# Performance work log

Hardware: AMD Instinct MI355X
Metric: run time of the kernel (lower is better)

## Reference

```python
import jax, jax.numpy as jnp
import numpy as np

# dims (match init_kwargs / input_specs)
B, T = 32, 512
DIM, DEPTH, HEADS, NB_FEAT, N_MASKS = 256, 6, 8, 128, 4
DIM_HEAD = DIM // HEADS  # 32
FF_MULT = 4
KERNEL_EPS = 1e-4


def _orth_proj(key, m, d):
    # FAVOR+ gaussian orthogonal random features: stacked QR blocks, row norms from fresh gaussians
    nb = m // d
    keys = jax.random.split(key, nb + 1)
    blocks = []
    for i in range(nb):
        g = jax.random.normal(keys[i], (d, d))
        q, _ = jnp.linalg.qr(g)
        blocks.append(q.T)
    proj = jnp.concatenate(blocks, axis=0)  # (m, d)
    norms = jnp.linalg.norm(jax.random.normal(keys[-1], (m, d)), axis=-1)
    return (proj * norms[:, None]).astype(jnp.float32)


def setup_inputs() -> dict:
    key = jax.random.key(0)
    ks = jax.random.split(key, 12)
    init = lambda k, sh: (jax.random.normal(k, sh, dtype=jnp.float32) * 0.02)
    L = DEPTH
    return {
        "mel": jax.random.normal(ks[0], (B, DIM, T), dtype=jnp.float32),
        "proj": _orth_proj(ks[1], NB_FEAT, DIM_HEAD),
        "ln1_g": jnp.ones((L, DIM), jnp.float32), "ln1_b": jnp.zeros((L, DIM), jnp.float32),
        "Wq": init(ks[2], (L, DIM, DIM)), "Wk": init(ks[3], (L, DIM, DIM)),
        "Wv": init(ks[4], (L, DIM, DIM)),
        "Wo": init(ks[5], (L, DIM, DIM)), "bo": jnp.zeros((L, DIM), jnp.float32),
        "ln2_g": jnp.ones((L, DIM), jnp.float32), "ln2_b": jnp.zeros((L, DIM), jnp.float32),
        "W1": init(ks[6], (L, DIM, FF_MULT * DIM)), "b1": jnp.zeros((L, FF_MULT * DIM), jnp.float32),
        "W2": init(ks[7], (L, FF_MULT * DIM, DIM)), "b2": jnp.zeros((L, DIM), jnp.float32),
        "Wm": init(ks[8], (DIM, N_MASKS)), "bm": jnp.zeros((N_MASKS,), jnp.float32),
    }


def _ln(x, g, b):
    mu = jnp.mean(x, -1, keepdims=True)
    var = jnp.var(x, -1, keepdims=True)
    return (x - mu) * jax.lax.rsqrt(var + 1e-5) * g + b


def _softmax_kernel(x, proj, is_query):
    # x: (B,H,N,dh), proj: (m,dh)
    dn = x.shape[-1] ** -0.25
    ratio = proj.shape[0] ** -0.5
    xd = jnp.einsum('bhnd,md->bhnm', x * dn, proj)
    diag = 0.5 * jnp.sum(jnp.square(x * dn), axis=-1, keepdims=True)
    if is_query:
        mx = jnp.max(xd, axis=-1, keepdims=True)
    else:
        mx = jnp.max(xd, axis=(-1, -2), keepdims=True)
    return ratio * (jnp.exp(xd - diag - mx) + KERNEL_EPS)


def _split_heads(x):
    b, n, _ = x.shape
    return x.reshape(b, n, HEADS, DIM_HEAD).transpose(0, 2, 1, 3)  # (B,H,N,dh)


def _forward(mel, proj, ln1_g, ln1_b, Wq, Wk, Wv, Wo, bo, ln2_g, ln2_b, W1, b1, W2, b2, Wm, bm):
    x = jnp.transpose(mel, (0, 2, 1))  # (B, T, DIM)
    for l in range(DEPTH):
        # --- FAVOR+ self-attention (pre-LN, non-causal linear attention) ---
        h = _ln(x, ln1_g[l], ln1_b[l])
        q = _split_heads(h @ Wq[l])
        k = _split_heads(h @ Wk[l])
        v = _split_heads(h @ Wv[l])
        qp = _softmax_kernel(q, proj, True)   # (B,H,T,m)
        kp = _softmax_kernel(k, proj, False)  # (B,H,T,m)
        ctx = jnp.einsum('bhnm,bhnd->bhmd', kp, v)          # (B,H,m,dh)
        o = jnp.einsum('bhnm,bhmd->bhnd', qp, ctx)          # (B,H,T,dh)
        denom = jnp.einsum('bhnm,bhm->bhn', qp, kp.sum(axis=2))
        o = o / denom[..., None]
        o = o.transpose(0, 2, 1, 3).reshape(x.shape[0], x.shape[1], DIM)
        x = x + o @ Wo[l] + bo[l]
        h = _ln(x, ln2_g[l], ln2_b[l])
        x = x + jax.nn.gelu(h @ W1[l] + b1[l]) @ W2[l] + b2[l]
    masks = x @ Wm + bm                  # (B, T, M)
    return jnp.transpose(masks, (0, 2, 1))  # (B, M, T)


def reference(mel, proj, ln1_g, ln1_b, Wq, Wk, Wv, Wo, bo, ln2_g, ln2_b, W1, b1, W2, b2, Wm, bm):
    return _forward(mel, proj, ln1_g, ln1_b, Wq, Wk, Wv, Wo, bo, ln2_g, ln2_b, W1, b1, W2, b2, Wm, bm)
```

## Files before the change

kernel.cpp:

```cpp
#include <hip/hip_runtime.h>
#include <math.h>

#define B 32
#define T 512
#define D 256
#define H 8
#define DH 32
#define MF 128
#define NLAYER 6
#define FF 1024
#define NM 4
#define BT (B*T)
#define BH (B*H)

#define DN2H 0.08838834764831845f
#define DNS  0.4204482076268573f
#define RATIO 0.08838834764831845f
#define KEPS 1e-4f

typedef __attribute__((ext_vector_type(8))) short short8;
typedef __attribute__((ext_vector_type(4))) float f32x4;

#define MFMA(a, b, c) __builtin_amdgcn_mfma_f32_16x16x32_bf16(a, b, c, 0, 0, 0)

#define SWZG(l) (((((l) & 3) + (((l) >> 3) & 3)) & 3) * 8)
#define RS(li, gi) (((((gi) - ((li) >> 1)) & 3)) * 8)

__device__ __forceinline__ ushort f2b(float x) {
  union { float f; unsigned u; } c; c.f = x;
  unsigned r = (c.u + 0x7FFFu + ((c.u >> 16) & 1u)) >> 16;
  return (ushort)r;
}
__device__ __forceinline__ float bf2f(ushort u) {
  union { unsigned u; float f; } c; c.u = ((unsigned)u) << 16;
  return c.f;
}
__device__ __forceinline__ void gload16(const ushort* g, ushort* l) {
  __builtin_amdgcn_global_load_lds((const __attribute__((address_space(1))) void*)g,
                                   (__attribute__((address_space(3))) void*)l, 16, 0, 0);
}

__global__ void transpose_mel(const float* __restrict__ mel, float* __restrict__ x) {
  __shared__ float tile[32][33];
  int b = blockIdx.z;
  int d0 = blockIdx.y * 32, t0 = blockIdx.x * 32;
  int tx = threadIdx.x, ty = threadIdx.y;
  #pragma unroll
  for (int i = 0; i < 32; i += 8)
    tile[ty + i][tx] = mel[(b * D + d0 + ty + i) * T + t0 + tx];
  __syncthreads();
  #pragma unroll
  for (int i = 0; i < 32; i += 8)
    x[(b * T + t0 + ty + i) * D + d0 + tx] = tile[tx][ty + i];
}

__global__ void wtrans(const float* __restrict__ W, ushort* __restrict__ WT,
                       int K, int N, size_t lin, size_t lout) {
  __shared__ float tile[32][33];
  int l = blockIdx.z;
// ... 11 lines not shown
}

__global__ void proj_conv(const float* __restrict__ proj, ushort* __restrict__ projd) {
  int e = blockIdx.x * 256 + threadIdx.x;
  if (e < MF * DH) projd[e] = f2b(proj[e] * DNS);
}

__global__ __launch_bounds__(256) void ln_kernel(const float* __restrict__ x, const float* __restrict__ g,
                          const float* __restrict__ bb, ushort* __restrict__ y) {
  int row = blockIdx.x * 4 + (threadIdx.x >> 6);
  int lane = threadIdx.x & 63;
  const float4 v = ((const float4*)(x + (size_t)row * D))[lane];
  float s = v.x + v.y + v.z + v.w;
  #pragma unroll
  for (int off = 32; off; off >>= 1) s += __shfl_down(s, off);
  s = __shfl(s, 0);
  float mu = s * (1.0f / 256.0f);
  float dx = v.x - mu, dy = v.y - mu, dz = v.z - mu, dw = v.w - mu;
  float q = dx * dx + dy * dy + dz * dz + dw * dw;
  #pragma unroll
  for (int off = 32; off; off >>= 1) q += __shfl_down(q, off);
  q = __shfl(q, 0);
  float rstd = rsqrtf(q * (1.0f / 256.0f) + 1e-5f);
  const float4 gg = ((const float4*)g)[lane];
  const float4 be = ((const float4*)bb)[lane];
  ushort4 o;
  o.x = f2b(dx * rstd * gg.x + be.x);
  o.y = f2b(dy * rstd * gg.y + be.y);
  o.z = f2b(dz * rstd * gg.z + be.z);
  o.w = f2b(dw * rstd * gg.w + be.w);
  ((ushort4*)(y + (size_t)row * D))[lane] = o;
}

template<int EPI, int BM>
__global__ __launch_bounds__(256) void gemm_bf16(
    const ushort* __restrict__ A, const ushort* __restrict__ BTm,
    const float* __restrict__ bias,
    ushort* __restrict__ outB,
    ushort* __restrict__ qo, ushort* __restrict__ ko, ushort* __restrict__ vT,
    int N, int K) {
  constexpr int MFR = BM / 32;
  __shared__ __align__(16) ushort Al[2][BM * 32];
  __shared__ __align__(16) ushort Bl[2][128 * 32];
  int tid = threadIdx.x;
  int wave = tid >> 6, lane = tid & 63;
  int wr = wave >> 1, wc = wave & 1;
  int gi = lane >> 4, li = lane & 15;
  int lrow = lane >> 2, lkb = SWZG(lane);
  int row0 = blockIdx.y * BM, col0 = blockIdx.x * 128;
  f32x4 acc[MFR][4] = {};

  auto stage = [&](int buf, int kk) {
    #pragma unroll
    for (int i = 0; i < BM / 64; i++) {
      int chunk = wave * (BM / 64) + i;
      gload16(&A[(size_t)(row0 + chunk * 16 + lrow) * K + kk + lkb], &Al[buf][chunk * 512]);
    }
    #pragma unroll
    for (int i = 0; i < 2; i++) {
      int chunk = wave * 2 + i;
      gload16(&BTm[(size_t)(col0 + chunk * 16 + lrow) * K + kk + lkb], &Bl[buf][chunk * 512]);
    }
  };

  stage(0, 0);
  __syncthreads();
  int cur = 0;
  for (int k0 = 0; k0 < K; k0 += 32, cur ^= 1) {
    if (k0 + 32 < K) stage(cur ^ 1, k0 + 32);
    short8 a[MFR], b[4];
    #pragma unroll
    for (int m = 0; m < MFR; m++)
      a[m] = *(const short8*)&Al[cur][(wr * (MFR * 16) + m * 16 + li) * 32 + RS(li, gi)];
    #pragma unroll
    for (int n = 0; n < 4; n++)
      b[n] = *(const short8*)&Bl[cur][(wc * 64 + n * 16 + li) * 32 + RS(li, gi)];
    #pragma unroll
    for (int m = 0; m < MFR; m++)
      #pragma unroll
      for (int n = 0; n < 4; n++)
        acc[m][n] = MFMA(a[m], b[n], acc[m][n]);
    __syncthreads();
  }
  #pragma unroll
  for (int m = 0; m < MFR; m++) {
    int rbase = row0 + wr * (MFR * 16) + m * 16 + gi * 4;
    #pragma unroll
    for (int n = 0; n < 4; n++) {
      int col = col0 + wc * 64 + n * 16 + li;
      f32x4 v = acc[m][n];
      if (EPI == 2) {
        float bs = bias[col];
        #pragma unroll
        for (int r = 0; r < 4; r++) {
          float u = v[r] + bs;
          float p = u + 0.044715f * u * u * u;
          float gel = u / (1.0f + __expf(-1.5957691216057308f * p));
          outB[(size_t)(rbase + r) * N + col] = f2b(gel);
        }
      } else {
        if (col < 256) {
          #pragma unroll
          for (int r = 0; r < 4; r++) qo[(size_t)(rbase + r) * 256 + col] = f2b(v[r]);
        } else if (col < 512) {
          #pragma unroll
          for (int r = 0; r < 4; r++) ko[(size_t)(rbase + r) * 256 + col - 256] = f2b(v[r]);
        } else {
          int b_ = rbase >> 9, t = rbase & 511;
          int hh = (col - 512) >> 5, d = (col - 512) & 31;
          ushort4 pk;
          pk.x = f2b(v[0]); pk.y = f2b(v[1]); pk.z = f2b(v[2]); pk.w = f2b(v[3]);
          *(ushort4*)&vT[((size_t)((b_ * 8 + hh) * 32 + d)) * 512 + t] = pk;
        }
      }
    }
  }
}

__global__ __launch_bounds__(256) void ctx_fused(
    const ushort* __restrict__ kb, const ushort* __restrict__ projd,
    const ushort* __restrict__ vT, ushort* __restrict__ Bmat) {
  __shared__ __align__(16) ushort Kl[512 * 32];
  __shared__ __align__(16) ushort Pl[128 * 32];
  __shared__ __align__(16) ushort Sl[2][128 * 40];
  __shared__ __align__(16) ushort Bvl[2][32 * 32];
  __shared__ float dg_s[512];
  __shared__ float red_s[256];
  int bh = blockIdx.x;
  int b = bh >> 3, h = bh & 7;
  int tid = threadIdx.x, wave = tid >> 6, lane = tid & 63;
  int gi = lane >> 4, li = lane & 15;
  int lrow = lane >> 2, lkb = (lane & 3) * 8;
  const ushort* Kg = kb + (size_t)(b * 512) * 256 + h * 32;
  const ushort* Vg = vT + (size_t)bh * 32 * 512;
  #pragma unroll
  for (int i = 0; i < 8; i++) {
    int chunk = wave * 8 + i;
    gload16(&Kg[(size_t)(chunk * 16 + lrow) * 256 + lkb], &Kl[chunk * 512]);
  }
  #pragma unroll
  for (int i = 0; i < 2; i++) {
    int chunk = wave * 2 + i;
    gload16(&projd[(chunk * 16 + lrow) * 32 + lkb], &Pl[chunk * 512]);
  }
  __syncthreads();
  #pragma unroll
  for (int i = 0; i < 2; i++) {
    int t = tid * 2 + i;
    const ushort* kr = &Kl[t * 32];
    float s = 0.f;
    #pragma unroll
    for (int j = 0; j < 32; j++) { float v = bf2f(kr[j]); s += v * v; }
    dg_s[t] = DN2H * s;
  }
  short8 bp0 = *(const short8*)&Pl[(wave * 32 + li) * 32 + gi * 8];
  short8 bp1 = *(const short8*)&Pl[(wave * 32 + 16 + li) * 32 + gi * 8];
  float smax = -1e30f;
  for (int c = 0; c < 16; c++) {
    int t0c = c * 32;
    short8 a0 = *(const short8*)&Kl[(t0c + li) * 32 + gi * 8];
    short8 a1 = *(const short8*)&Kl[(t0c + 16 + li) * 32 + gi * 8];
    f32x4 s00 = {}, s01 = {}, s10 = {}, s11 = {};
    s00 = MFMA(a0, bp0, s00); s01 = MFMA(a0, bp1, s01);
    s10 = MFMA(a1, bp0, s10); s11 = MFMA(a1, bp1, s11);
    #pragma unroll
    for (int r = 0; r < 4; r++)
      smax = fmaxf(smax, fmaxf(fmaxf(s00[r], s01[r]), fmaxf(s10[r], s11[r])));
  }
  red_s[tid] = smax;
  __syncthreads();
  for (int s = 128; s; s >>= 1) {
    if (tid < s) red_s[tid] = fmaxf(red_s[tid], red_s[tid + s]);
    __syncthreads();
  }
  float km = red_s[0];
  f32x4 cacc[2][2] = {};
  float ks0 = 0.f, ks1 = 0.f;
  int cur = 0;
  for (int c = 0; c < 16; c++, cur ^= 1) {
    int t0c = c * 32;
    if (wave < 2)
      gload16(&Vg[(size_t)(wave * 16 + lrow) * 512 + t0c + lkb], &Bvl[cur][wave * 512]);
    short8 a0 = *(const short8*)&Kl[(t0c + li) * 32 + gi * 8];
    short8 a1 = *(const short8*)&Kl[(t0c + 16 + li) * 32 + gi * 8];
    f32x4 s00 = {}, s01 = {}, s10 = {}, s11 = {};
    s00 = MFMA(a0, bp0, s00); s01 = MFMA(a0, bp1, s01);
    s10 = MFMA(a1, bp0, s10); s11 = MFMA(a1, bp1, s11);
    ushort4 w00, w01, w10, w11;
    #pragma unroll
    for (int r = 0; r < 4; r++) {
      float d0 = dg_s[t0c + gi * 4 + r];
      float d1 = dg_s[t0c + 16 + gi * 4 + r];
      float k00 = RATIO * (__expf(s00[r] - d0 - km) + KEPS);
      float k01 = RATIO * (__expf(s01[r] - d0 - km) + KEPS);
      float k10 = RATIO * (__expf(s10[r] - d1 - km) + KEPS);
      float k11 = RATIO * (__expf(s11[r] - d1 - km) + KEPS);
      ks0 += k00 + k10; ks1 += k01 + k11;
      ((ushort*)&w00)[r] = f2b(k00); ((ushort*)&w01)[r] = f2b(k01);
      ((ushort*)&w10)[r] = f2b(k10); ((ushort*)&w11)[r] = f2b(k11);
    }
    *(ushort4*)&Sl[cur][(wave * 32 + li) * 40 + gi * 4]           = w00;
    *(ushort4*)&Sl[cur][(wave * 32 + 16 + li) * 40 + gi * 4]      = w01;
    *(ushort4*)&Sl[cur][(wave * 32 + li) * 40 + 16 + gi * 4]      = w10;
    *(ushort4*)&Sl[cur][(wave * 32 + 16 + li) * 40 + 16 + gi * 4] = w11;
    __syncthreads();
    short8 ca0 = *(const short8*)&Sl[cur][(wave * 32 + li) * 40 + gi * 8];
    short8 ca1 = *(const short8*)&Sl[cur][(wave * 32 + 16 + li) * 40 + gi * 8];
    short8 cb0 = *(const short8*)&Bvl[cur][li * 32 + gi * 8];
    short8 cb1 = *(const short8*)&Bvl[cur][(16 + li) * 32 + gi * 8];
    cacc[0][0] = MFMA(ca0, cb0, cacc[0][0]);
    cacc[0][1] = MFMA(ca0, cb1, cacc[0][1]);
    cacc[1][0] = MFMA(ca1, cb0, cacc[1][0]);
    cacc[1][1] = MFMA(ca1, cb1, cacc[1][1]);
  }
  ks0 += __shfl_xor(ks0, 16); ks0 += __shfl_xor(ks0, 32);
  ks1 += __shfl_xor(ks1, 16); ks1 += __shfl_xor(ks1, 32);
  if (gi == 0) {
    Bmat[((size_t)bh * 48 + 32) * 128 + wave * 32 + li] = f2b(ks0);
    Bmat[((size_t)bh * 48 + 32) * 128 + wave * 32 + 16 + li] = f2b(ks1);
  }
  #pragma unroll
  for (int m = 0; m < 2; m++)
    #pragma unroll
    for (int n = 0; n < 2; n++) {
      int dd = n * 16 + li;
      int mg = wave * 32 + m * 16 + gi * 4;
      ushort4 pk;
      pk.x = f2b(cacc[m][n][0]); pk.y = f2b(cacc[m][n][1]);
      pk.z = f2b(cacc[m][n][2]); pk.w = f2b(cacc[m][n][3]);
      *(ushort4*)&Bmat[((size_t)bh * 48 + dd) * 128 + mg] = pk;
    }
  for (int e = tid; e < 15 * 128; e += 256)
    Bmat[((size_t)bh * 48 + 33) * 128 + e] = 0;
}

__global__ __launch_bounds__(256) void favq_o(
    const ushort* __restrict__ qb, const ushort* __restrict__ projd,
    const ushort* __restrict__ Bmat, ushort* __restrict__ ob) {
  __shared__ __align__(16) ushort Ql[64 * 32];
  __shared__ __align__(16) ushort Pl[128 * 32];
  __shared__ __align__(16) ushort Sl[64 * 136];
  __shared__ __align__(16) ushort Bml[48 * 136];
  __shared__ float dgq[64];
  int bh = blockIdx.y;
  int t0 = blockIdx.x * 64;
  int b = bh >> 3, h = bh & 7;
  int tid = threadIdx.x, wave = tid >> 6, lane = tid & 63;
  int gi = lane >> 4, li = lane & 15;
  int lrow = lane >> 2, lkb = (lane & 3) * 8;
  const ushort* Qg = qb + (size_t)(b * 512) * 256 + h * 32;
  gload16(&Qg[(size_t)(t0 + wave * 16 + lrow) * 256 + lkb], &Ql[wave * 512]);
  #pragma unroll
  for (int i = 0; i < 2; i++) {
    int chunk = wave * 2 + i;
    gload16(&projd[(chunk * 16 + lrow) * 32 + lkb], &Pl[chunk * 512]);
  }
  #pragma unroll
  for (int j = 0; j < 3; j++) {
    int c = j * 256 + tid;
    int r = c >> 4, g = c & 15;
    *(uint4*)&Bml[r * 136 + g * 8] = *(const uint4*)&Bmat[(size_t)bh * 48 * 128 + r * 128 + g * 8];
  }
  __syncthreads();
  if (tid < 64) {
    const ushort* qr = &Ql[tid * 32];
// ... 18 lines not shown
  mx = fmaxf(mx, __shfl_xor(mx, 16));
  mx = fmaxf(mx, __shfl_xor(mx, 32));
  float dg = dgq[wave * 16 + li];
  #pragma unroll
  for (int m = 0; m < 8; m++) {
    ushort4 o4;
    #pragma unroll
    for (int r = 0; r < 4; r++)
      ((ushort*)&o4)[r] = f2b(RATIO * (__expf(sacc[m][r] - dg - mx) + KEPS));
    *(ushort4*)&Sl[(wave * 16 + li) * 136 + m * 16 + gi * 4] = o4;
  }
  __syncthreads();
  f32x4 oacc[3] = {};
  #pragma unroll
  for (int ks = 0; ks < 4; ks++) {
    short8 a = *(const short8*)&Sl[(wave * 16 + li) * 136 + ks * 32 + gi * 8];
    #pragma unroll
    for (int n = 0; n < 3; n++) {
      short8 bb = *(const short8*)&Bml[(n * 16 + li) * 136 + ks * 32 + gi * 8];
      oacc[n] = MFMA(a, bb, oacc[n]);
    }
  }
  int t = t0 + wave * 16 + gi * 4;
  float den[4];
  #pragma unroll
  for (int r = 0; r < 4; r++) den[r] = __shfl(oacc[2][r], lane & 48);
  #pragma unroll
  for (int n = 0; n < 2; n++)
    #pragma unroll
    for (int r = 0; r < 4; r++)
      ob[((size_t)(b * 512) + t + r) * 256 + h * 32 + n * 16 + li] = f2b(oacc[n][r] / den[r]);
}

template<int MODE>
__global__ __launch_bounds__(256) void gemm_ln2(
    const ushort* __restrict__ A, const ushort* __restrict__ BTm,
    const float* __restrict__ bias, const float* __restrict__ res,
    float* __restrict__ x, const float* __restrict__ g, const float* __restrict__ bvec,
    ushort* __restrict__ hout,
    const float* __restrict__ Wm, const float* __restrict__ bm, float* __restrict__ mout,
    int K) {
  __shared__ __align__(16) ushort Al[2][32 * 32];
  __shared__ __align__(16) ushort Bl[2][256 * 32];
  __shared__ float rs1[4 * 32];
  __shared__ float rs2[4 * 32];
  __shared__ float pmS[4 * 128];
  int tid = threadIdx.x, wave = tid >> 6, lane = tid & 63;
  int gi = lane >> 4, li = lane & 15;
  int lrow = lane >> 2, lkb = SWZG(lane);
  int row0 = blockIdx.x * 32;
  int wc = wave;
  f32x4 acc[2][4] = {};

  auto stage = [&](int buf, int kk) {
    if (wave < 2)
      gload16(&A[(size_t)(row0 + wave * 16 + lrow) * K + kk + lkb], &Al[buf][wave * 512]);
    #pragma unroll
    for (int i = 0; i < 4; i++) {
      int chunk = wave * 4 + i;
      gload16(&BTm[(size_t)(chunk * 16 + lrow) * K + kk + lkb], &Bl[buf][chunk * 512]);
    }
  };

  stage(0, 0);
  __syncthreads();
  int cur = 0;
  for (int k0 = 0; k0 < K; k0 += 32, cur ^= 1) {
    if (k0 + 32 < K) stage(cur ^ 1, k0 + 32);
    short8 a[2], b[4];
    #pragma unroll
    for (int m = 0; m < 2; m++)
      a[m] = *(const short8*)&Al[cur][(m * 16 + li) * 32 + RS(li, gi)];
    #pragma unroll
    for (int n = 0; n < 4; n++)
      b[n] = *(const short8*)&Bl[cur][(wc * 64 + n * 16 + li) * 32 + RS(li, gi)];
    #pragma unroll
    for (int m = 0; m < 2; m++)
      #pragma unroll
      for (int n = 0; n < 4; n++)
        acc[m][n] = MFMA(a[m], b[n], acc[m][n]);
    __syncthreads();
  }
  #pragma unroll
  for (int m = 0; m < 2; m++) {
    #pragma unroll
    for (int r = 0; r < 4; r++) {
      int row = row0 + m * 16 + gi * 4 + r;
      int ridx = m * 16 + gi * 4 + r;
      float s1 = 0.f, s2 = 0.f;
      #pragma unroll
      for (int n = 0; n < 4; n++) {
        int col = wc * 64 + n * 16 + li;
        float val = acc[m][n][r] + bias[col] + res[(size_t)row * 256 + col];
        acc[m][n][r] = val;
        s1 += val; s2 += val * val;
      }
      if (MODE == 0) {
        #pragma unroll
        for (int off = 1; off <= 8; off <<= 1) { s1 += __shfl_xor(s1, off); s2 += __shfl_xor(s2, off); }
        if (li == 0) { rs1[wave * 32 + ridx] = s1; rs2[wave * 32 + ridx] = s2; }
      } else {
        #pragma unroll
        for (int msk = 0; msk < NM; msk++) {
          float sm = 0.f;
          #pragma unroll
          for (int n = 0; n < 4; n++) {
            int col = wc * 64 + n * 16 + li;
            sm += acc[m][n][r] * Wm[col * NM + msk];
          }
          #pragma unroll
          for (int off = 1; off <= 8; off <<= 1) sm += __shfl_xor(sm, off);
          if (li == 0) pmS[wave * 128 + ridx * 4 + msk] = sm;
        }
      }
    }
  }
  __syncthreads();
  if (MODE == 0) {
    float g4[4], bv4[4];
    #pragma unroll
    for (int n = 0; n < 4; n++) {
      int col = wc * 64 + n * 16 + li;
      g4[n] = g[col]; bv4[n] = bvec[col];
    }
    #pragma unroll
    for (int m = 0; m < 2; m++) {
      #pragma unroll
      for (int r = 0; r < 4; r++) {
        int row = row0 + m * 16 + gi * 4 + r;
        int ridx = m * 16 + gi * 4 + r;
        float t1 = rs1[ridx] + rs1[32 + ridx] + rs1[64 + ridx] + rs1[96 + ridx];
        float t2 = rs2[ridx] + rs2[32 + ridx] + rs2[64 + ridx] + rs2[96 + ridx];
        float mu = t1 * (1.f / 256.f);
        float rstd = rsqrtf(t2 * (1.f / 256.f) - mu * mu + 1e-5f);
        #pragma unroll
        for (int n = 0; n < 4; n++) {
          int col = wc * 64 + n * 16 + li;
          float val = acc[m][n][r];
          x[(size_t)row * 256 + col] = val;
          hout[(size_t)row * 256 + col] = f2b((val - mu) * rstd * g4[n] + bv4[n]);
        }
      }
    }
  } else {
    if (tid < 128) {
      int ridx = tid >> 2, msk = tid & 3;
      float tot = pmS[ridx * 4 + msk] + pmS[128 + ridx * 4 + msk] +
                  pmS[256 + ridx * 4 + msk] + pmS[384 + ridx * 4 + msk];
      int grow = row0 + ridx;
      int bb_ = grow >> 9, t = grow & 511;
      mout[((size_t)(bb_ * NM) + msk) * 512 + t] = tot + bm[msk];
    }
  }
}

extern "C" void kernel_launch(void* const* d_in, const int* in_sizes, int n_in,
                              void* d_out, int out_size, void* d_ws, size_t ws_size,
                              hipStream_t stream) {
  const float* mel   = (const float*)d_in[0];
  const float* proj  = (const float*)d_in[1];
  const float* ln1_g = (const float*)d_in[2];
  const float* ln1_b = (const float*)d_in[3];
  const float* Wq    = (const float*)d_in[4];
  const float* Wk    = (const float*)d_in[5];
  const float* Wv    = (const float*)d_in[6];
  const float* Wo    = (const float*)d_in[7];
  const float* bo    = (const float*)d_in[8];
  const float* ln2_g = (const float*)d_in[9];
  const float* ln2_b = (const float*)d_in[10];
  const float* W1    = (const float*)d_in[11];
  const float* b1    = (const float*)d_in[12];
  const float* W2    = (const float*)d_in[13];
  const float* b2    = (const float*)d_in[14];
  const float* Wm    = (const float*)d_in[15];
  const float* bm    = (const float*)d_in[16];

  float* x      = (float*)d_ws;
  ushort* us    = (ushort*)(x + (size_t)BT * D);
  ushort* h     = us;                   us += (size_t)BT * D;
  ushort* qb    = us;                   us += (size_t)BT * D;
  ushort* kb    = us;                   us += (size_t)BT * D;
  ushort* vT    = us;                   us += (size_t)BH * 32 * T;
  ushort* ob    = us;                   us += (size_t)BT * D;
  ushort* ffh   = us;                   us += (size_t)BT * FF;
  ushort* Bmat  = us;                   us += (size_t)BH * 48 * MF;
  ushort* qkvT  = us;                   us += (size_t)NLAYER * 768 * 256;
  ushort* woT   = us;                   us += (size_t)NLAYER * 256 * 256;
  ushort* w1T   = us;                   us += (size_t)NLAYER * 1024 * 256;
  ushort* w2T   = us;                   us += (size_t)NLAYER * 256 * 1024;
  ushort* projd = us;                   us += (size_t)MF * DH;

  wtrans<<<dim3(8, 8, NLAYER), dim3(32, 8), 0, stream>>>(Wq, qkvT, 256, 256, 65536, 768 * 256);
  wtrans<<<dim3(8, 8, NLAYER), dim3(32, 8), 0, stream>>>(Wk, qkvT + 256 * 256, 256, 256, 65536, 768 * 256);
  wtrans<<<dim3(8, 8, NLAYER), dim3(32, 8), 0, stream>>>(Wv, qkvT + 512 * 256, 256, 256, 65536, 768 * 256);
  wtrans<<<dim3(8, 8, NLAYER), dim3(32, 8), 0, stream>>>(Wo, woT, 256, 256, 65536, 65536);
  wtrans<<<dim3(32, 8, NLAYER), dim3(32, 8), 0, stream>>>(W1, w1T, 256, 1024, 262144, 262144);
  wtrans<<<dim3(8, 32, NLAYER), dim3(32, 8), 0, stream>>>(W2, w2T, 1024, 256, 262144, 262144);
  proj_conv<<<16, 256, 0, stream>>>(proj, projd);

  transpose_mel<<<dim3(T / 32, D / 32, B), dim3(32, 8), 0, stream>>>(mel, x);
  ln_kernel<<<BT / 4, 256, 0, stream>>>(x, ln1_g, ln1_b, h);

  for (int l = 0; l < NLAYER; l++) {
    gemm_bf16<0, 64><<<dim3(6, 256), 256, 0, stream>>>(h, qkvT + (size_t)l * 768 * 256,
        nullptr, nullptr, qb, kb, vT, 768, 256);
    ctx_fused<<<BH, 256, 0, stream>>>(kb, projd, vT, Bmat);
    favq_o<<<dim3(8, BH), 256, 0, stream>>>(qb, projd, Bmat, ob);
    gemm_ln2<0><<<BT / 32, 256, 0, stream>>>(ob, woT + (size_t)l * 256 * 256,
        bo + l * D, x, x, ln2_g + l * D, ln2_b + l * D, h,
        nullptr, nullptr, nullptr, 256);
    gemm_bf16<2, 64><<<dim3(8, 256), 256, 0, stream>>>(h, w1T + (size_t)l * 1024 * 256,
        b1 + (size_t)l * FF, ffh, nullptr, nullptr, nullptr, 1024, 256);
    if (l < NLAYER - 1) {
      gemm_ln2<0><<<BT / 32, 256, 0, stream>>>(ffh, w2T + (size_t)l * 256 * 1024,
          b2 + l * D, x, x, ln1_g + (l + 1) * D, ln1_b + (l + 1) * D, h,
          nullptr, nullptr, nullptr, 1024);
    } else {
      gemm_ln2<1><<<BT / 32, 256, 0, stream>>>(ffh, w2T + (size_t)l * 256 * 1024,
          b2 + l * D, x, x, nullptr, nullptr, nullptr,
          Wm, bm, (float*)d_out, 1024);
    }
  }
}
```

Baseline: 750.0 us.

## Use 32x256 GEMM tiles with row-major grid and widen ctx_fused to 512 threads

Replaces the 64x128 GEMM tile with a 32x256 tile in which each wave owns a 64-column slice and all waves share the A rows. The grid is reordered so blockIdx.x walks rows, letting consecutive blocks share the same weight columns. ctx_fused moves from 256 to 512 threads, each wave handling 16 feature columns instead of 32, so per-wave work drops and each (b,h) block gets more parallelism. The trade-offs are less A reuse per B tile, fewer MFMAs per LDS load in the GEMM, and more barrier participants in ctx_fused.

```diff
diff --git a/kernel.cpp b/kernel.cpp
--- a/kernel.cpp
+++ b/kernel.cpp
@@ -102,33 +102,28 @@
   ((ushort4*)(y + (size_t)row * D))[lane] = o;
 }
 
-template<int EPI, int BM>
-__global__ __launch_bounds__(256) void gemm_bf16(
+template<int EPI>
+__global__ __launch_bounds__(256) void gemm_wide(
     const ushort* __restrict__ A, const ushort* __restrict__ BTm,
     const float* __restrict__ bias,
     ushort* __restrict__ outB,
     ushort* __restrict__ qo, ushort* __restrict__ ko, ushort* __restrict__ vT,
     int N, int K) {
-  constexpr int MFR = BM / 32;
-  __shared__ __align__(16) ushort Al[2][BM * 32];
-  __shared__ __align__(16) ushort Bl[2][128 * 32];
+  __shared__ __align__(16) ushort Al[2][32 * 32];
+  __shared__ __align__(16) ushort Bl[2][256 * 32];
   int tid = threadIdx.x;
   int wave = tid >> 6, lane = tid & 63;
-  int wr = wave >> 1, wc = wave & 1;
   int gi = lane >> 4, li = lane & 15;
   int lrow = lane >> 2, lkb = SWZG(lane);
-  int row0 = blockIdx.y * BM, col0 = blockIdx.x * 128;
-  f32x4 acc[MFR][4] = {};
+  int row0 = blockIdx.x * 32, col0 = blockIdx.y * 256;
+  f32x4 acc[2][4] = {};
 
   auto stage = [&](int buf, int kk) {
-    #pragma unroll
-    for (int i = 0; i < BM / 64; i++) {
-      int chunk = wave * (BM / 64) + i;
-      gload16(&A[(size_t)(row0 + chunk * 16 + lrow) * K + kk + lkb], &Al[buf][chunk * 512]);
-    }
-    #pragma unroll
-    for (int i = 0; i < 2; i++) {
-      int chunk = wave * 2 + i;
+    if (wave < 2)
+      gload16(&A[(size_t)(row0 + wave * 16 + lrow) * K + kk + lkb], &Al[buf][wave * 512]);
+    #pragma unroll
+    for (int i = 0; i < 4; i++) {
+      int chunk = wave * 4 + i;
       gload16(&BTm[(size_t)(col0 + chunk * 16 + lrow) * K + kk + lkb], &Bl[buf][chunk * 512]);
     }
   };
@@ -138,26 +133,26 @@
   int cur = 0;
   for (int k0 = 0; k0 < K; k0 += 32, cur ^= 1) {
     if (k0 + 32 < K) stage(cur ^ 1, k0 + 32);
-    short8 a[MFR], b[4];
-    #pragma unroll
-    for (int m = 0; m < MFR; m++)
-      a[m] = *(const short8*)&Al[cur][(wr * (MFR * 16) + m * 16 + li) * 32 + RS(li, gi)];
+    short8 a[2], b[4];
+    #pragma unroll
+    for (int m = 0; m < 2; m++)
+      a[m] = *(const short8*)&Al[cur][(m * 16 + li) * 32 + RS(li, gi)];
     #pragma unroll
     for (int n = 0; n < 4; n++)
-      b[n] = *(const short8*)&Bl[cur][(wc * 64 + n * 16 + li) * 32 + RS(li, gi)];
-    #pragma unroll
-    for (int m = 0; m < MFR; m++)
+      b[n] = *(const short8*)&Bl[cur][(wave * 64 + n * 16 + li) * 32 + RS(li, gi)];
+    #pragma unroll
+    for (int m = 0; m < 2; m++)
       #pragma unroll
       for (int n = 0; n < 4; n++)
         acc[m][n] = MFMA(a[m], b[n], acc[m][n]);
     __syncthreads();
   }
   #pragma unroll
-  for (int m = 0; m < MFR; m++) {
-    int rbase = row0 + wr * (MFR * 16) + m * 16 + gi * 4;
+  for (int m = 0; m < 2; m++) {
+    int rbase = row0 + m * 16 + gi * 4;
     #pragma unroll
     for (int n = 0; n < 4; n++) {
-      int col = col0 + wc * 64 + n * 16 + li;
+      int col = col0 + wave * 64 + n * 16 + li;
       f32x4 v = acc[m][n];
       if (EPI == 2) {
         float bs = bias[col];
@@ -187,7 +182,7 @@
   }
 }
 
-__global__ __launch_bounds__(256) void ctx_fused(
+__global__ __launch_bounds__(512) void ctx_fused(
     const ushort* __restrict__ kb, const ushort* __restrict__ projd,
     const ushort* __restrict__ vT, ushort* __restrict__ Bmat) {
   __shared__ __align__(16) ushort Kl[512 * 32];
@@ -195,7 +190,7 @@
   __shared__ __align__(16) ushort Sl[2][128 * 40];
   __shared__ __align__(16) ushort Bvl[2][32 * 32];
   __shared__ float dg_s[512];
-  __shared__ float red_s[256];
+  __shared__ float red_s[512];
   int bh = blockIdx.x;
   int b = bh >> 3, h = bh & 7;
   int tid = threadIdx.x, wave = tid >> 6, lane = tid & 63;
@@ -204,48 +199,40 @@
   const ushort* Kg = kb + (size_t)(b * 512) * 256 + h * 32;
   const ushort* Vg = vT + (size_t)bh * 32 * 512;
   #pragma unroll
-  for (int i = 0; i < 8; i++) {
-    int chunk = wave * 8 + i;
+  for (int i = 0; i < 4; i++) {
+    int chunk = wave * 4 + i;
     gload16(&Kg[(size_t)(chunk * 16 + lrow) * 256 + lkb], &Kl[chunk * 512]);
   }
-  #pragma unroll
-  for (int i = 0; i < 2; i++) {
-    int chunk = wave * 2 + i;
-    gload16(&projd[(chunk * 16 + lrow) * 32 + lkb], &Pl[chunk * 512]);
-  }
-  __syncthreads();
-  #pragma unroll
-  for (int i = 0; i < 2; i++) {
-    int t = tid * 2 + i;
-    const ushort* kr = &Kl[t * 32];
+  gload16(&projd[(wave * 16 + lrow) * 32 + lkb], &Pl[wave * 512]);
+  __syncthreads();
+  {
+    const ushort* kr = &Kl[tid * 32];
     float s = 0.f;
     #pragma unroll
     for (int j = 0; j < 32; j++) { float v = bf2f(kr[j]); s += v * v; }
-    dg_s[t] = DN2H * s;
-  }
-  short8 bp0 = *(const short8*)&Pl[(wave * 32 + li) * 32 + gi * 8];
-  short8 bp1 = *(const short8*)&Pl[(wave * 32 + 16 + li) * 32 + gi * 8];
+    dg_s[tid] = DN2H * s;
+  }
+  short8 bp = *(const short8*)&Pl[(wave * 16 + li) * 32 + gi * 8];
   float smax = -1e30f;
   for (int c = 0; c < 16; c++) {
     int t0c = c * 32;
     short8 a0 = *(const short8*)&Kl[(t0c + li) * 32 + gi * 8];
     short8 a1 = *(const short8*)&Kl[(t0c + 16 + li) * 32 + gi * 8];
-    f32x4 s00 = {}, s01 = {}, s10 = {}, s11 = {};
-    s00 = MFMA(a0, bp0, s00); s01 = MFMA(a0, bp1, s01);
-    s10 = MFMA(a1, bp0, s10); s11 = MFMA(a1, bp1, s11);
+    f32x4 s0 = {}, s1 = {};
+    s0 = MFMA(a0, bp, s0); s1 = MFMA(a1, bp, s1);
     #pragma unroll
     for (int r = 0; r < 4; r++)
-      smax = fmaxf(smax, fmaxf(fmaxf(s00[r], s01[r]), fmaxf(s10[r], s11[r])));
+      smax = fmaxf(smax, fmaxf(s0[r], s1[r]));
   }
   red_s[tid] = smax;
   __syncthreads();
-  for (int s = 128; s; s >>= 1) {
+  for (int s = 256; s; s >>= 1) {
     if (tid < s) red_s[tid] = fmaxf(red_s[tid], red_s[tid + s]);
     __syncthreads();
   }
   float km = red_s[0];
-  f32x4 cacc[2][2] = {};
-  float ks0 = 0.f, ks1 = 0.f;
+  f32x4 cacc[2] = {};
+  float ks = 0.f;
   int cur = 0;
   for (int c = 0; c < 16; c++, cur ^= 1) {
     int t0c = c * 32;
@@ -253,54 +240,41 @@
       gload16(&Vg[(size_t)(wave * 16 + lrow) * 512 + t0c + lkb], &Bvl[cur][wave * 512]);
     short8 a0 = *(const short8*)&Kl[(t0c + li) * 32 + gi * 8];
     short8 a1 = *(const short8*)&Kl[(t0c + 16 + li) * 32 + gi * 8];
-    f32x4 s00 = {}, s01 = {}, s10 = {}, s11 = {};
-    s00 = MFMA(a0, bp0, s00); s01 = MFMA(a0, bp1, s01);
-    s10 = MFMA(a1, bp0, s10); s11 = MFMA(a1, bp1, s11);
-    ushort4 w00, w01, w10, w11;
+    f32x4 s0 = {}, s1 = {};
+    s0 = MFMA(a0, bp, s0); s1 = MFMA(a1, bp, s1);
+    ushort4 w0, w1;
     #pragma unroll
     for (int r = 0; r < 4; r++) {
       float d0 = dg_s[t0c + gi * 4 + r];
       float d1 = dg_s[t0c + 16 + gi * 4 + r];
-      float k00 = RATIO * (__expf(s00[r] - d0 - km) + KEPS);
-      float k01 = RATIO * (__expf(s01[r] - d0 - km) + KEPS);
-      float k10 = RATIO * (__expf(s10[r] - d1 - km) + KEPS);
-      float k11 = RATIO * (__expf(s11[r] - d1 - km) + KEPS);
-      ks0 += k00 + k10; ks1 += k01 + k11;
-      ((ushort*)&w00)[r] = f2b(k00); ((ushort*)&w01)[r] = f2b(k01);
-      ((ushort*)&w10)[r] = f2b(k10); ((ushort*)&w11)[r] = f2b(k11);
-    }
-    *(ushort4*)&Sl[cur][(wave * 32 + li) * 40 + gi * 4]           = w00;
-    *(ushort4*)&Sl[cur][(wave * 32 + 16 + li) * 40 + gi * 4]      = w01;
-    *(ushort4*)&Sl[cur][(wave * 32 + li) * 40 + 16 + gi * 4]      = w10;
-    *(ushort4*)&Sl[cur][(wave * 32 + 16 + li) * 40 + 16 + gi * 4] = w11;
+      float k0 = RATIO * (__expf(s0[r] - d0 - km) + KEPS);
+      float k1 = RATIO * (__expf(s1[r] - d1 - km) + KEPS);
+      ks += k0 + k1;
+      ((ushort*)&w0)[r] = f2b(k0);
+      ((ushort*)&w1)[r] = f2b(k1);
+    }
+    *(ushort4*)&Sl[cur][(wave * 16 + li) * 40 + gi * 4]      = w0;
+    *(ushort4*)&Sl[cur][(wave * 16 + li) * 40 + 16 + gi * 4] = w1;
     __syncthreads();
-    short8 ca0 = *(const short8*)&Sl[cur][(wave * 32 + li) * 40 + gi * 8];
-    short8 ca1 = *(const short8*)&Sl[cur][(wave * 32 + 16 + li) * 40 + gi * 8];
+    short8 ca = *(const short8*)&Sl[cur][(wave * 16 + li) * 40 + gi * 8];
     short8 cb0 = *(const short8*)&Bvl[cur][li * 32 + gi * 8];
     short8 cb1 = *(const short8*)&Bvl[cur][(16 + li) * 32 + gi * 8];
-    cacc[0][0] = MFMA(ca0, cb0, cacc[0][0]);
-    cacc[0][1] = MFMA(ca0, cb1, cacc[0][1]);
-    cacc[1][0] = MFMA(ca1, cb0, cacc[1][0]);
-    cacc[1][1] = MFMA(ca1, cb1, cacc[1][1]);
-  }
-  ks0 += __shfl_xor(ks0, 16); ks0 += __shfl_xor(ks0, 32);
-  ks1 += __shfl_xor(ks1, 16); ks1 += __shfl_xor(ks1, 32);
-  if (gi == 0) {
-    Bmat[((size_t)bh * 48 + 32) * 128 + wave * 32 + li] = f2b(ks0);
-    Bmat[((size_t)bh * 48 + 32) * 128 + wave * 32 + 16 + li] = f2b(ks1);
-  }
-  #pragma unroll
-  for (int m = 0; m < 2; m++)
-    #pragma unroll
-    for (int n = 0; n < 2; n++) {
-      int dd = n * 16 + li;
-      int mg = wave * 32 + m * 16 + gi * 4;
-      ushort4 pk;
-      pk.x = f2b(cacc[m][n][0]); pk.y = f2b(cacc[m][n][1]);
-      pk.z = f2b(cacc[m][n][2]); pk.w = f2b(cacc[m][n][3]);
-      *(ushort4*)&Bmat[((size_t)bh * 48 + dd) * 128 + mg] = pk;
-    }
-  for (int e = tid; e < 15 * 128; e += 256)
+    cacc[0] = MFMA(ca, cb0, cacc[0]);
+    cacc[1] = MFMA(ca, cb1, cacc[1]);
+  }
+  ks += __shfl_xor(ks, 16); ks += __shfl_xor(ks, 32);
+  if (gi == 0)
+    Bmat[((size_t)bh * 48 + 32) * 128 + wave * 16 + li] = f2b(ks);
+  #pragma unroll
+  for (int n = 0; n < 2; n++) {
+    int dd = n * 16 + li;
+    int mg = wave * 16 + gi * 4;
+    ushort4 pk;
+    pk.x = f2b(cacc[n][0]); pk.y = f2b(cacc[n][1]);
+    pk.z = f2b(cacc[n][2]); pk.w = f2b(cacc[n][3]);
+    *(ushort4*)&Bmat[((size_t)bh * 48 + dd) * 128 + mg] = pk;
+  }
+  for (int e = tid; e < 15 * 128; e += 512)
     Bmat[((size_t)bh * 48 + 33) * 128 + e] = 0;
 }
 
@@ -555,14 +529,14 @@
   ln_kernel<<<BT / 4, 256, 0, stream>>>(x, ln1_g, ln1_b, h);
 
   for (int l = 0; l < NLAYER; l++) {
-    gemm_bf16<0, 64><<<dim3(6, 256), 256, 0, stream>>>(h, qkvT + (size_t)l * 768 * 256,
+    gemm_wide<0><<<dim3(BT / 32, 3), 256, 0, stream>>>(h, qkvT + (size_t)l * 768 * 256,
         nullptr, nullptr, qb, kb, vT, 768, 256);
-    ctx_fused<<<BH, 256, 0, stream>>>(kb, projd, vT, Bmat);
+    ctx_fused<<<BH, 512, 0, stream>>>(kb, projd, vT, Bmat);
     favq_o<<<dim3(8, BH), 256, 0, stream>>>(qb, projd, Bmat, ob);
     gemm_ln2<0><<<BT / 32, 256, 0, stream>>>(ob, woT + (size_t)l * 256 * 256,
         bo + l * D, x, x, ln2_g + l * D, ln2_b + l * D, h,
         nullptr, nullptr, nullptr, 256);
-    gemm_bf16<2, 64><<<dim3(8, 256), 256, 0, stream>>>(h, w1T + (size_t)l * 1024 * 256,
+    gemm_wide<2><<<dim3(BT / 32, 4), 256, 0, stream>>>(h, w1T + (size_t)l * 1024 * 256,
         b1 + (size_t)l * FF, ffh, nullptr, nullptr, nullptr, 1024, 256);
     if (l < NLAYER - 1) {
       gemm_ln2<0><<<BT / 32, 256, 0, stream>>>(ffh, w2T + (size_t)l * 256 * 1024,
```

After: 759.2 us. No clear change (+1.2%).

## Fuse Wo+LN2+FF1 and FF2+LN1+QKV GEMMs keeping normalized rows in LDS

Applied to the files above, without the earlier changes.

Merges the output projection, residual, LayerNorm and FF1 GELU GEMM into one kernel, and FF2, residual, next-layer LayerNorm and QKV projection into another. The normalized activations stay in swizzled shared memory instead of going through global memory, which removes two launches per layer and the h round trip. The generic GEMM also swaps __syncthreads for explicit vmcnt waits plus raw barriers. Each fused block now recomputes across all 1024 or 768 output columns with only 512 blocks, so parallelism per launch drops and shared memory use rises.

```diff
diff --git a/kernel.cpp b/kernel.cpp
--- a/kernel.cpp
+++ b/kernel.cpp
@@ -25,6 +25,8 @@
 
 #define SWZG(l) (((((l) & 3) + (((l) >> 3) & 3)) & 3) * 8)
 #define RS(li, gi) (((((gi) - ((li) >> 1)) & 3)) * 8)
+
+#define WAIT_VM(N) asm volatile("s_waitcnt vmcnt(" #N ")" ::: "memory")
 
 __device__ __forceinline__ ushort f2b(float x) {
   union { float f; unsigned u; } c; c.f = x;
@@ -134,10 +136,16 @@
   };
 
   stage(0, 0);
-  __syncthreads();
   int cur = 0;
   for (int k0 = 0; k0 < K; k0 += 32, cur ^= 1) {
-    if (k0 + 32 < K) stage(cur ^ 1, k0 + 32);
+    if (k0 + 32 < K) {
+      stage(cur ^ 1, k0 + 32);
+      if (BM == 64) { WAIT_VM(3); } else { WAIT_VM(4); }
+    } else {
+      WAIT_VM(0);
+    }
+    __builtin_amdgcn_s_barrier();
+    __builtin_amdgcn_sched_barrier(0);
     short8 a[MFR], b[4];
     #pragma unroll
     for (int m = 0; m < MFR; m++)
@@ -150,7 +158,7 @@
       #pragma unroll
       for (int n = 0; n < 4; n++)
         acc[m][n] = MFMA(a[m], b[n], acc[m][n]);
-    __syncthreads();
+    __builtin_amdgcn_s_barrier();
   }
   #pragma unroll
   for (int m = 0; m < MFR; m++) {
@@ -385,18 +393,311 @@
       ob[((size_t)(b * 512) + t + r) * 256 + h * 32 + n * 16 + li] = f2b(oacc[n][r] / den[r]);
 }
 
-template<int MODE>
-__global__ __launch_bounds__(256) void gemm_ln2(
+__global__ __launch_bounds__(256) void wo_ff1(
+    const ushort* __restrict__ ob, const ushort* __restrict__ woT,
+    const float* __restrict__ bo, const float* __restrict__ res, float* __restrict__ x,
+    const float* __restrict__ g, const float* __restrict__ bvec,
+    const ushort* __restrict__ w1T, const float* __restrict__ b1v,
+    ushort* __restrict__ ffh) {
+  __shared__ __align__(16) ushort Al[2][32 * 32];
+  __shared__ __align__(16) ushort Bl[2][256 * 32];
+  __shared__ __align__(16) ushort Hp[8 * 1024];
+  __shared__ float rs1[4 * 32], rs2[4 * 32];
+  int tid = threadIdx.x, wave = tid >> 6, lane = tid & 63;
+  int gi = lane >> 4, li = lane & 15;
+  int lrow = lane >> 2, lkb = SWZG(lane);
+  int row0 = blockIdx.x * 32;
+  int wc = wave;
+  f32x4 acc[2][4] = {};
+
+  auto stage1 = [&](int buf, int kk) {
+    if (wave < 2)
+      gload16(&ob[(size_t)(row0 + wave * 16 + lrow) * 256 + kk + lkb], &Al[buf][wave * 512]);
+    #pragma unroll
+    for (int i = 0; i < 4; i++) {
+      int chunk = wave * 4 + i;
+      gload16(&woT[(size_t)(chunk * 16 + lrow) * 256 + kk + lkb], &Bl[buf][chunk * 512]);
+    }
+  };
+  stage1(0, 0);
+  __syncthreads();
+  int cur = 0;
+  for (int k0 = 0; k0 < 256; k0 += 32, cur ^= 1) {
+    if (k0 + 32 < 256) stage1(cur ^ 1, k0 + 32);
+    short8 a[2], b[4];
+    #pragma unroll
+    for (int m = 0; m < 2; m++)
+      a[m] = *(const short8*)&Al[cur][(m * 16 + li) * 32 + RS(li, gi)];
+    #pragma unroll
+    for (int n = 0; n < 4; n++)
+      b[n] = *(const short8*)&Bl[cur][(wc * 64 + n * 16 + li) * 32 + RS(li, gi)];
+    #pragma unroll
+    for (int m = 0; m < 2; m++)
+      #pragma unroll
+      for (int n = 0; n < 4; n++)
+        acc[m][n] = MFMA(a[m], b[n], acc[m][n]);
+    __syncthreads();
+  }
+  #pragma unroll
+  for (int m = 0; m < 2; m++) {
+    #pragma unroll
+    for (int r = 0; r < 4; r++) {
+      int row = row0 + m * 16 + gi * 4 + r;
+      int ridx = m * 16 + gi * 4 + r;
+      float s1 = 0.f, s2 = 0.f;
+      #pragma unroll
+      for (int n = 0; n < 4; n++) {
+        int col = wc * 64 + n * 16 + li;
+        float val = acc[m][n][r] + bo[col] + res[(size_t)row * 256 + col];
+        acc[m][n][r] = val;
+        s1 += val; s2 += val * val;
+      }
+      #pragma unroll
+      for (int off = 1; off <= 8; off <<= 1) { s1 += __shfl_xor(s1, off); s2 += __shfl_xor(s2, off); }
+      if (li == 0) { rs1[wave * 32 + ridx] = s1; rs2[wave * 32 + ridx] = s2; }
+    }
+  }
+  __syncthreads();
+  {
+    float g4[4], bv4[4];
+    #pragma unroll
+    for (int n = 0; n < 4; n++) {
+      int col = wc * 64 + n * 16 + li;
+      g4[n] = g[col]; bv4[n] = bvec[col];
+    }
+    #pragma unroll
+    for (int m = 0; m < 2; m++) {
+      #pragma unroll
+      for (int r = 0; r < 4; r++) {
+        int row32 = m * 16 + gi * 4 + r;
+        int row = row0 + row32;
+        float t1 = rs1[row32] + rs1[32 + row32] + rs1[64 + row32] + rs1[96 + row32];
+        float t2 = rs2[row32] + rs2[32 + row32] + rs2[64 + row32] + rs2[96 + row32];
+        float mu = t1 * (1.f / 256.f);
+        float rstd = rsqrtf(t2 * (1.f / 256.f) - mu * mu + 1e-5f);
+        #pragma unroll
+        for (int n = 0; n < 4; n++) {
+          int col = wc * 64 + n * 16 + li;
+          float val = acc[m][n][r];
+          x[(size_t)row * 256 + col] = val;
+          float hv = (val - mu) * rstd * g4[n] + bv4[n];
+          int kc = col >> 5, c32 = col & 31;
+          int G = c32 >> 3, c7 = c32 & 7;
+          int slot = (G - (row32 >> 1)) & 3;
+          Hp[kc * 1024 + row32 * 32 + slot * 8 + c7] = f2b(hv);
+        }
+      }
+    }
+  }
+  auto stage2 = [&](int buf, int st) {
+    int nc = st >> 3, ks = st & 7;
+    #pragma unroll
+    for (int i = 0; i < 4; i++) {
+      int chunk = wave * 4 + i;
+      gload16(&w1T[(size_t)(nc * 256 + chunk * 16 + lrow) * 256 + ks * 32 + lkb], &Bl[buf][chunk * 512]);
+    }
+  };
+  stage2(0, 0);
+  __syncthreads();
+  cur = 0;
+  f32x4 fac[2][4] = {};
+  for (int st = 0; st < 32; st++, cur ^= 1) {
+    int nc = st >> 3, ks = st & 7;
+    if (st + 1 < 32) stage2(cur ^ 1, st + 1);
+    short8 a[2], b[4];
+    #pragma unroll
+    for (int m = 0; m < 2; m++)
+      a[m] = *(const short8*)&Hp[ks * 1024 + (m * 16 + li) * 32 + RS(li, gi)];
+    #pragma unroll
+    for (int n = 0; n < 4; n++)
+      b[n] = *(const short8*)&Bl[cur][(wc * 64 + n * 16 + li) * 32 + RS(li, gi)];
+    #pragma unroll
+    for (int m = 0; m < 2; m++)
+      #pragma unroll
+      for (int n = 0; n < 4; n++)
+        fac[m][n] = MFMA(a[m], b[n], fac[m][n]);
+    if (ks == 7) {
+      #pragma unroll
+      for (int m = 0; m < 2; m++) {
+        int rbase = row0 + m * 16 + gi * 4;
+        #pragma unroll
+        for (int n = 0; n < 4; n++) {
+          int col = nc * 256 + wc * 64 + n * 16 + li;
+          float bs = b1v[col];
+          #pragma unroll
+          for (int r = 0; r < 4; r++) {
+            float u = fac[m][n][r] + bs;
+            float p = u + 0.044715f * u * u * u;
+            float gel = u / (1.0f + __expf(-1.5957691216057308f * p));
+            ffh[(size_t)(rbase + r) * 1024 + col] = f2b(gel);
+            fac[m][n][r] = 0.f;
+          }
+        }
+      }
+    }
+    __syncthreads();
+  }
+}
+
+__global__ __launch_bounds__(256) void ff2_qkv(
+    const ushort* __restrict__ ffh, const ushort* __restrict__ w2T,
+    const float* __restrict__ b2v, const float* __restrict__ res, float* __restrict__ x,
+    const float* __restrict__ g, const float* __restrict__ bvec,
+    const ushort* __restrict__ qkvT,
+    ushort* __restrict__ qo, ushort* __restrict__ ko, ushort* __restrict__ vT) {
+  __shared__ __align__(16) ushort Al[2][32 * 32];
+  __shared__ __align__(16) ushort Bl[2][256 * 32];
+  __shared__ __align__(16) ushort Hp[8 * 1024];
+  __shared__ float rs1[4 * 32], rs2[4 * 32];
+  int tid = threadIdx.x, wave = tid >> 6, lane = tid & 63;
+  int gi = lane >> 4, li = lane & 15;
+  int lrow = lane >> 2, lkb = SWZG(lane);
+  int row0 = blockIdx.x * 32;
+  int wc = wave;
+  f32x4 acc[2][4] = {};
+
+  auto stage1 = [&](int buf, int kk) {
+    if (wave < 2)
+      gload16(&ffh[(size_t)(row0 + wave * 16 + lrow) * 1024 + kk + lkb], &Al[buf][wave * 512]);
+    #pragma unroll
+    for (int i = 0; i < 4; i++) {
+      int chunk = wave * 4 + i;
+      gload16(&w2T[(size_t)(chunk * 16 + lrow) * 1024 + kk + lkb], &Bl[buf][chunk * 512]);
+    }
+  };
+  stage1(0, 0);
+  __syncthreads();
+  int cur = 0;
+  for (int k0 = 0; k0 < 1024; k0 += 32, cur ^= 1) {
+    if (k0 + 32 < 1024) stage1(cur ^ 1, k0 + 32);
+    short8 a[2], b[4];
+    #pragma unroll
+    for (int m = 0; m < 2; m++)
+      a[m] = *(const short8*)&Al[cur][(m * 16 + li) * 32 + RS(li, gi)];
+    #pragma unroll
+    for (int n = 0; n < 4; n++)
+      b[n] = *(const short8*)&Bl[cur][(wc * 64 + n * 16 + li) * 32 + RS(li, gi)];
+    #pragma unroll
+    for (int m = 0; m < 2; m++)
+      #pragma unroll
+      for (int n = 0; n < 4; n++)
+        acc[m][n] = MFMA(a[m], b[n], acc[m][n]);
+    __syncthreads();
+  }
+  #pragma unroll
+  for (int m = 0; m < 2; m++) {
+    #pragma unroll
+    for (int r = 0; r < 4; r++) {
+      int row = row0 + m * 16 + gi * 4 + r;
+      int ridx = m * 16 + gi * 4 + r;
+      float s1 = 0.f, s2 = 0.f;
+      #pragma unroll
+      for (int n = 0; n < 4; n++) {
+        int col = wc * 64 + n * 16 + li;
+        float val = acc[m][n][r] + b2v[col] + res[(size_t)row * 256 + col];
+        acc[m][n][r] = val;
+        s1 += val; s2 += val * val;
+      }
+      #pragma unroll
+      for (int off = 1; off <= 8; off <<= 1) { s1 += __shfl_xor(s1, off); s2 += __shfl_xor(s2, off); }
+      if (li == 0) { rs1[wave * 32 + ridx] = s1; rs2[wave * 32 + ridx] = s2; }
+    }
+  }
+  __syncthreads();
+  {
+    float g4[4], bv4[4];
+    #pragma unroll
+    for (int n = 0; n < 4; n++) {
+      int col = wc * 64 + n * 16 + li;
+      g4[n] = g[col]; bv4[n] = bvec[col];
+    }
+    #pragma unroll
+    for (int m = 0; m < 2; m++) {
+      #pragma unroll
+      for (int r = 0; r < 4; r++) {
+        int row32 = m * 16 + gi * 4 + r;
+        int row = row0 + row32;
+        float t1 = rs1[row32] + rs1[32 + row32] + rs1[64 + row32] + rs1[96 + row32];
+        float t2 = rs2[row32] + rs2[32 + row32] + rs2[64 + row32] + rs2[96 + row32];
+        float mu = t1 * (1.f / 256.f);
+        float rstd = rsqrtf(t2 * (1.f / 256.f) - mu * mu + 1e-5f);
+        #pragma unroll
+        for (int n = 0; n < 4; n++) {
+          int col = wc * 64 + n * 16 + li;
+          float val = acc[m][n][r];
+          x[(size_t)row * 256 + col] = val;
+          float hv = (val - mu) * rstd * g4[n] + bv4[n];
+          int kc = col >> 5, c32 = col & 31;
+          int G = c32 >> 3, c7 = c32 & 7;
+          int slot = (G - (row32 >> 1)) & 3;
+          Hp[kc * 1024 + row32 * 32 + slot * 8 + c7] = f2b(hv);
+        }
+      }
+    }
+  }
+  auto stage2 = [&](int buf, int st) {
+    int nc = st >> 3, ks = st & 7;
+    #pragma unroll
+    for (int i = 0; i < 4; i++) {
+      int chunk = wave * 4 + i;
+      gload16(&qkvT[(size_t)(nc * 256 + chunk * 16 + lrow) * 256 + ks * 32 + lkb], &Bl[buf][chunk * 512]);
+    }
+  };
+  stage2(0, 0);
+  __syncthreads();
+  cur = 0;
+  f32x4 fac[2][4] = {};
+  for (int st = 0; st < 24; st++, cur ^= 1) {
+    int nc = st >> 3, ks = st & 7;
+    if (st + 1 < 24) stage2(cur ^ 1, st + 1);
+    short8 a[2], b[4];
+    #pragma unroll
+    for (int m = 0; m < 2; m++)
+      a[m] = *(const short8*)&Hp[ks * 1024 + (m * 16 + li) * 32 + RS(li, gi)];
+    #pragma unroll
+    for (int n = 0; n < 4; n++)
+      b[n] = *(const short8*)&Bl[cur][(wc * 64 + n * 16 + li) * 32 + RS(li, gi)];
+    #pragma unroll
+    for (int m = 0; m < 2; m++)
+      #pragma unroll
+      for (int n = 0; n < 4; n++)
+        fac[m][n] = MFMA(a[m], b[n], fac[m][n]);
+    if (ks == 7) {
+      #pragma unroll
+      for (int m = 0; m < 2; m++) {
+        int rbase = row0 + m * 16 + gi * 4;
+        #pragma unroll
+        for (int n = 0; n < 4; n++) {
+          int col256 = wc * 64 + n * 16 + li;
+          if (nc == 0) {
+            #pragma unroll
+            for (int r = 0; r < 4; r++) { qo[(size_t)(rbase + r) * 256 + col256] = f2b(fac[m][n][r]); fac[m][n][r] = 0.f; }
+          } else if (nc == 1) {
+            #pragma unroll
+            for (int r = 0; r < 4; r++) { ko[(size_t)(rbase + r) * 256 + col256] = f2b(fac[m][n][r]); fac[m][n][r] = 0.f; }
+          } else {
+            int b_ = rbase >> 9, t = rbase & 511;
+            int hh = col256 >> 5, d = col256 & 31;
+            ushort4 pk;
+            pk.x = f2b(fac[m][n][0]); pk.y = f2b(fac[m][n][1]);
+            pk.z = f2b(fac[m][n][2]); pk.w = f2b(fac[m][n][3]);
+            *(ushort4*)&vT[((size_t)((b_ * 8 + hh) * 32 + d)) * 512 + t] = pk;
+            fac[m][n][0] = fac[m][n][1] = fac[m][n][2] = fac[m][n][3] = 0.f;
+          }
+        }
+      }
+    }
+    __syncthreads();
+  }
+}
+
+__global__ __launch_bounds__(256) void gemm_mask(
     const ushort* __restrict__ A, const ushort* __restrict__ BTm,
     const float* __restrict__ bias, const float* __restrict__ res,
-    float* __restrict__ x, const float* __restrict__ g, const float* __restrict__ bvec,
-    ushort* __restrict__ hout,
     const float* __restrict__ Wm, const float* __restrict__ bm, float* __restrict__ mout,
     int K) {
   __shared__ __align__(16) ushort Al[2][32 * 32];
   __shared__ __align__(16) ushort Bl[2][256 * 32];
-  __shared__ float rs1[4 * 32];
-  __shared__ float rs2[4 * 32];
   __shared__ float pmS[4 * 128];
   int tid = threadIdx.x, wave = tid >> 6, lane = tid & 63;
   int gi = lane >> 4, li = lane & 15;
@@ -414,7 +715,6 @@
       gload16(&BTm[(size_t)(chunk * 16 + lrow) * K + kk + lkb], &Bl[buf][chunk * 512]);
     }
   };
-
   stage(0, 0);
   __syncthreads();
   int cur = 0;
@@ -440,70 +740,33 @@
     for (int r = 0; r < 4; r++) {
       int row = row0 + m * 16 + gi * 4 + r;
       int ridx = m * 16 + gi * 4 + r;
-      float s1 = 0.f, s2 = 0.f;
       #pragma unroll
       for (int n = 0; n < 4; n++) {
         int col = wc * 64 + n * 16 + li;
-        float val = acc[m][n][r] + bias[col] + res[(size_t)row * 256 + col];
-        acc[m][n][r] = val;
-        s1 += val; s2 += val * val;
+        acc[m][n][r] += bias[col] + res[(size_t)row * 256 + col];
       }
-      if (MODE == 0) {
-        #pragma unroll
-        for (int off = 1; off <= 8; off <<= 1) { s1 += __shfl_xor(s1, off); s2 += __shfl_xor(s2, off); }
-        if (li == 0) { rs1[wave * 32 + ridx] = s1; rs2[wave * 32 + ridx] = s2; }
-      } else {
-        #pragma unroll
-        for (int msk = 0; msk < NM; msk++) {
-          float sm = 0.f;
-          #pragma unroll
-          for (int n = 0; n < 4; n++) {
-            int col = wc * 64 + n * 16 + li;
-            sm += acc[m][n][r] * Wm[col * NM + msk];
-          }
-          #pragma unroll
-          for (int off = 1; off <= 8; off <<= 1) sm += __shfl_xor(sm, off);
-          if (li == 0) pmS[wave * 128 + ridx * 4 + msk] = sm;
-        }
-      }
-    }
-  }
-  __syncthreads();
-  if (MODE == 0) {
-    float g4[4], bv4[4];
-    #pragma unroll
-    for (int n = 0; n < 4; n++) {
-      int col = wc * 64 + n * 16 + li;
-      g4[n] = g[col]; bv4[n] = bvec[col];
-    }
-    #pragma unroll
-    for (int m = 0; m < 2; m++) {
-      #pragma unroll
-      for (int r = 0; r < 4; r++) {
-        int row = row0 + m * 16 + gi * 4 + r;
-        int ridx = m * 16 + gi * 4 + r;
-        float t1 = rs1[ridx] + rs1[32 + ridx] + rs1[64 + ridx] + rs1[96 + ridx];
-        float t2 = rs2[ridx] + rs2[32 + ridx] + rs2[64 + ridx] + rs2[96 + ridx];
-        float mu = t1 * (1.f / 256.f);
-        float rstd = rsqrtf(t2 * (1.f / 256.f) - mu * mu + 1e-5f);
+      #pragma unroll
+      for (int msk = 0; msk < NM; msk++) {
+        float sm = 0.f;
         #pragma unroll
         for (int n = 0; n < 4; n++) {
           int col = wc * 64 + n * 16 + li;
-          float val = acc[m][n][r];
-          x[(size_t)row * 256 + col] = val;
-          hout[(size_t)row * 256 + col] = f2b((val - mu) * rstd * g4[n] + bv4[n]);
+          sm += acc[m][n][r] * Wm[col * NM + msk];
         }
+        #pragma unroll
+        for (int off = 1; off <= 8; off <<= 1) sm += __shfl_xor(sm, off);
+        if (li == 0) pmS[wave * 128 + ridx * 4 + msk] = sm;
       }
     }
-  } else {
-    if (tid < 128) {
-      int ridx = tid >> 2, msk = tid & 3;
-      float tot = pmS[ridx * 4 + msk] + pmS[128 + ridx * 4 + msk] +
-                  pmS[256 + ridx * 4 + msk] + pmS[384 + ridx * 4 + msk];
-      int grow = row0 + ridx;
-      int bb_ = grow >> 9, t = grow & 511;
-      mout[((size_t)(bb_ * NM) + msk) * 512 + t] = tot + bm[msk];
-    }
+  }
+  __syncthreads();
+  if (tid < 128) {
+    int ridx = tid >> 2, msk = tid & 3;
+    float tot = pmS[ridx * 4 + msk] + pmS[128 + ridx * 4 + msk] +
+                pmS[256 + ridx * 4 + msk] + pmS[384 + ridx * 4 + msk];
+    int grow = row0 + ridx;
+    int bb_ = grow >> 9, t = grow & 511;
+    mout[((size_t)(bb_ * NM) + msk) * 512 + t] = tot + bm[msk];
   }
 }
 
@@ -554,24 +817,22 @@
   transpose_mel<<<dim3(T / 32, D / 32, B), dim3(32, 8), 0, stream>>>(mel, x);
   ln_kernel<<<BT / 4, 256, 0, stream>>>(x, ln1_g, ln1_b, h);
 
+  gemm_bf16<0, 64><<<dim3(6, 256), 256, 0, stream>>>(h, qkvT,
+      nullptr, nullptr, qb, kb, vT, 768, 256);
+
   for (int l = 0; l < NLAYER; l++) {
-    gemm_bf16<0, 64><<<dim3(6, 256), 256, 0, stream>>>(h, qkvT + (size_t)l * 768 * 256,
-        nullptr, nullptr, qb, kb, vT, 768, 256);
     ctx_fused<<<BH, 256, 0, stream>>>(kb, projd, vT, Bmat);
     favq_o<<<dim3(8, BH), 256, 0, stream>>>(qb, projd, Bmat, ob);
-    gemm_ln2<0><<<BT / 32, 256, 0, stream>>>(ob, woT + (size_t)l * 256 * 256,
-        bo + l * D, x, x, ln2_g + l * D, ln2_b + l * D, h,
-        nullptr, nullptr, nullptr, 256);
-    gemm_bf16<2, 64><<<dim3(8, 256), 256, 0, stream>>>(h, w1T + (size_t)l * 1024 * 256,
-        b1 + (size_t)l * FF, ffh, nullptr, nullptr, nullptr, 1024, 256);
+    wo_ff1<<<BT / 32, 256, 0, stream>>>(ob, woT + (size_t)l * 256 * 256,
+        bo + l * D, x, x, ln2_g + l * D, ln2_b + l * D,
+        w1T + (size_t)l * 1024 * 256, b1 + (size_t)l * FF, ffh);
     if (l < NLAYER - 1) {
-      gemm_ln2<0><<<BT / 32, 256, 0, stream>>>(ffh, w2T + (size_t)l * 256 * 1024,
-          b2 + l * D, x, x, ln1_g + (l + 1) * D, ln1_b + (l + 1) * D, h,
-          nullptr, nullptr, nullptr, 1024);
+      ff2_qkv<<<BT / 32, 256, 0, stream>>>(ffh, w2T + (size_t)l * 256 * 1024,
+          b2 + l * D, x, x, ln1_g + (l + 1) * D, ln1_b + (l + 1) * D,
+          qkvT + (size_t)(l + 1) * 768 * 256, qb, kb, vT);
     } else {
-      gemm_ln2<1><<<BT / 32, 256, 0, stream>>>(ffh, w2T + (size_t)l * 256 * 1024,
-          b2 + l * D, x, x, nullptr, nullptr, nullptr,
-          Wm, bm, (float*)d_out, 1024);
-    }
-  }
-}
+      gemm_mask<<<BT / 32, 256, 0, stream>>>(ffh, w2T + (size_t)l * 256 * 1024,
+          b2 + l * D, x, Wm, bm, (float*)d_out, 1024);
+    }
+  }
+}
```

Result: faster. 724.7 us (-3.4%).
